# Optimization experiments

Measured on AMD Instinct MI355X. Metric: run time of the kernel, lower is better.

## Reference

```python
import jax, jax.numpy as jnp
import numpy as np
from jax import lax

D_MODEL = 1024
D_STATE = 16
D_CONV = 4
EXPAND = 2
D_INNER = EXPAND * D_MODEL  # 2048
DT_RANK = (D_MODEL + 15) // 16  # 64
EPS = 1e-5


def setup_inputs() -> dict:
    key = jax.random.key(0)
    ks = jax.random.split(key, 10)
    B, L = 2, 2048
    x = jax.random.normal(ks[0], (B, L, D_MODEL), dtype=jnp.float32)
    s = 0.02
    W_in = jax.random.normal(ks[1], (D_MODEL, 2 * D_INNER), dtype=jnp.float32) * s
    conv_w = jax.random.normal(ks[2], (D_INNER, 1, D_CONV), dtype=jnp.float32) * 0.3
    conv_b = jnp.zeros((D_INNER,), dtype=jnp.float32)
    W_xproj = jax.random.normal(ks[3], (D_INNER, DT_RANK + 2 * D_STATE), dtype=jnp.float32) * s
    W_dt = jax.random.normal(ks[4], (DT_RANK, D_INNER), dtype=jnp.float32) * s
    b_dt = jax.random.normal(ks[5], (D_INNER,), dtype=jnp.float32) * 0.1
    # canonical S4D-real init: A_log = log(1..d_state) broadcast over channels
    A_log = jnp.broadcast_to(jnp.log(jnp.arange(1, D_STATE + 1, dtype=jnp.float32)), (D_INNER, D_STATE))
    D = jnp.ones((D_INNER,), dtype=jnp.float32)
    W_out = jax.random.normal(ks[6], (D_INNER, D_MODEL), dtype=jnp.float32) * s
    return {
        'x': x,
        'ln_w': jnp.ones((D_MODEL,), dtype=jnp.float32),
        'ln_b': jnp.zeros((D_MODEL,), dtype=jnp.float32),
        'W_in': W_in, 'conv_w': conv_w, 'conv_b': conv_b,
        'W_xproj': W_xproj, 'W_dt': W_dt, 'b_dt': b_dt,
        'A_log': A_log, 'D': D, 'W_out': W_out,
    }


def _layernorm(x, w, b):
    mu = jnp.mean(x, axis=-1, keepdims=True)
    var = jnp.mean(jnp.square(x - mu), axis=-1, keepdims=True)
    return (x - mu) * lax.rsqrt(var + EPS) * w + b


def _mamba_forward(normed, W_in, conv_w, conv_b, W_xproj, W_dt, b_dt, A_log, D, W_out):
    Bsz, L, _ = normed.shape
    xz = normed @ W_in                       # (B, L, 2*d_inner)
    u, z = jnp.split(xz, 2, axis=-1)         # each (B, L, d_inner)
    # depthwise causal conv over time
    uc = lax.conv_general_dilated(
        jnp.swapaxes(u, 1, 2), conv_w,       # (B, d_inner, L), (d_inner, 1, k)
        window_strides=(1,), padding=[(D_CONV - 1, 0)],
        feature_group_count=D_INNER,
        dimension_numbers=('NCH', 'OIH', 'NCH'))
    uc = uc + conv_b[None, :, None]
    u = jax.nn.silu(jnp.swapaxes(uc, 1, 2))  # (B, L, d_inner)
    # input-dependent dt, B, C
    dbc = u @ W_xproj                        # (B, L, dt_rank + 2*d_state)
    dt = dbc[..., :DT_RANK]
    Bm = dbc[..., DT_RANK:DT_RANK + D_STATE]
    Cm = dbc[..., DT_RANK + D_STATE:]
    delta = jax.nn.softplus(dt @ W_dt + b_dt)  # (B, L, d_inner)
    A = -jnp.exp(A_log)                        # (d_inner, d_state)

    def step(h, inp):
        delta_t, u_t, B_t, C_t = inp           # (B,d), (B,d), (B,n), (B,n)
        dA = jnp.exp(delta_t[:, :, None] * A)  # (B, d, n)
        h = dA * h + (delta_t * u_t)[:, :, None] * B_t[:, None, :]
        y = jnp.einsum('bdn,bn->bd', h, C_t)
        return h, y

    tm = lambda a: jnp.swapaxes(a, 0, 1)       # time-major
    h0 = jnp.zeros((Bsz, D_INNER, D_STATE), dtype=normed.dtype)
    _, ys = lax.scan(step, h0, (tm(delta), tm(u), tm(Bm), tm(Cm)))
    y = jnp.swapaxes(ys, 0, 1) + u * D         # (B, L, d_inner)
    y = y * jax.nn.silu(z)
    return y @ W_out                            # (B, L, d_model)


def reference(x, ln_w, ln_b, W_in, conv_w, conv_b, W_xproj, W_dt, b_dt, A_log, D, W_out):
    normed = _layernorm(x, ln_w, ln_b)
    ssm_out = _mamba_forward(normed, W_in, conv_w, conv_b, W_xproj, W_dt, b_dt, A_log, D, W_out)
    # dropout is identity at inference
    return x + ssm_out
```

## Files before the change

### kernel.cpp

```cpp
#include <hip/hip_runtime.h>
#include <math.h>

#define D_MODEL 1024
#define D_INNER 2048
#define D_STATE 16
#define DT_RANK 64
#define LSEQ    2048
#define NTOK    4096
#define SCH     32
#define SCL     (LSEQ / SCH)
#define LOG2E   1.44269504088896f

typedef short bf16x8 __attribute__((ext_vector_type(8)));
typedef float f32x4  __attribute__((ext_vector_type(4)));

__device__ __forceinline__ unsigned bf16_rne(float v) {
    unsigned u = __float_as_uint(v);
    return (u + 0x7FFFu + ((u >> 16) & 1u)) >> 16;
}
__device__ __forceinline__ void split_hi_lo(float v, short& h, short& l) {
    unsigned hb = bf16_rne(v);
    h = (short)hb;
    float r = v - __uint_as_float(hb << 16);
    l = (short)bf16_rne(r);
}

__global__ __launch_bounds__(256) void ln_kernel(const float* __restrict__ x,
                                                 const float* __restrict__ w,
                                                 const float* __restrict__ b,
                                                 short* __restrict__ nh,
                                                 short* __restrict__ nl)
{
    int t = blockIdx.x;
    const float4* xr = (const float4*)(x + (size_t)t * D_MODEL);
    float4 v = xr[threadIdx.x];
    float s  = v.x + v.y + v.z + v.w;
    float s2 = v.x*v.x + v.y*v.y + v.z*v.z + v.w*v.w;
    for (int off = 32; off > 0; off >>= 1) {
        s  += __shfl_down(s, off);
        s2 += __shfl_down(s2, off);
    }
    __shared__ float red[8];
    int wid = threadIdx.x >> 6, lane = threadIdx.x & 63;
    if (lane == 0) { red[wid] = s; red[4 + wid] = s2; }
    __syncthreads();
    if (threadIdx.x == 0) {
        float a = red[0] + red[1] + red[2] + red[3];
        float c = red[4] + red[5] + red[6] + red[7];
        red[0] = a * (1.f / (float)D_MODEL);
        red[4] = c * (1.f / (float)D_MODEL);
    }
    __syncthreads();
    float mu  = red[0];
    float var = red[4] - mu * mu;
    float rs  = rsqrtf(var + 1e-5f);
    float4 wv = ((const float4*)w)[threadIdx.x];
    float4 bv = ((const float4*)b)[threadIdx.x];
    float4 o;
    o.x = (v.x - mu) * rs * wv.x + bv.x;
    o.y = (v.y - mu) * rs * wv.y + bv.y;
    o.z = (v.z - mu) * rs * wv.z + bv.z;
    o.w = (v.w - mu) * rs * wv.w + bv.w;
    short4 h4, l4;
    split_hi_lo(o.x, h4.x, l4.x);
    split_hi_lo(o.y, h4.y, l4.y);
    split_hi_lo(o.z, h4.z, l4.z);
    split_hi_lo(o.w, h4.w, l4.w);
    size_t off = (size_t)t * D_MODEL + threadIdx.x * 4;
    *(short4*)&nh[off] = h4;
    *(short4*)&nl[off] = l4;
}

__global__ __launch_bounds__(256) void cvtT_k(const float* __restrict__ W,
                                              short* __restrict__ Th,
                                              short* __restrict__ Tl,
                                              int R, int Cc)
{
    __shared__ float t[64][65];
    int rr = threadIdx.x >> 4;
    int cc = (threadIdx.x & 15) << 2;
    int r0 = blockIdx.y * 64, c0 = blockIdx.x * 64;
#pragma unroll
    for (int s = 0; s < 4; ++s) {
        float4 v = *(const float4*)&W[(size_t)(r0 + rr + 16*s) * Cc + c0 + cc];
        t[rr+16*s][cc+0] = v.x; t[rr+16*s][cc+1] = v.y;
        t[rr+16*s][cc+2] = v.z; t[rr+16*s][cc+3] = v.w;
    }
    __syncthreads();
#pragma unroll
    for (int s = 0; s < 4; ++s) {
        int orow = rr + 16*s;
        short4 h4, l4;
        split_hi_lo(t[cc+0][orow], h4.x, l4.x);
        split_hi_lo(t[cc+1][orow], h4.y, l4.y);
        split_hi_lo(t[cc+2][orow], h4.z, l4.z);
        split_hi_lo(t[cc+3][orow], h4.w, l4.w);
        size_t off = (size_t)(c0 + orow) * R + r0 + cc;
        *(short4*)&Th[off] = h4;
        *(short4*)&Tl[off] = l4;
    }
}

template<int EPI>
__global__ __launch_bounds__(256) void mgemm_k(const short* __restrict__ Ah,
                                               const short* __restrict__ Al,
                                               const short* __restrict__ Bh,
                                               const short* __restrict__ Bl,
                                               float* __restrict__ C, int ldc,
                                               int K, const float* __restrict__ aux)
{
    __shared__ short lds[4][128 * 32];

    int tid  = threadIdx.x;
    int w    = tid >> 6;
    int lane = tid & 63;
    int wr   = w >> 1, wc = w & 1;
    int row0 = blockIdx.y * 128;
    int col0 = blockIdx.x * 128;

    const short* gA = (w & 1) ? Al : Ah;
    const short* gB = (w & 1) ? Bl : Bh;
    const short* g  = (w & 2) ? gB : gA;
    int obase       = (w & 2) ? col0 : row0;
    const short* gtile = g + (size_t)obase * K;

    int srow  = lane >> 2;
    int skc   = lane & 3;
    int swoff = skc * 128 + srow * 8;

    int fr = lane & 15;
    int kg = lane >> 4;

    f32x4 acc[4][4] = {};

    for (int k0 = 0; k0 < K; k0 += 32) {
        bf16x8 stg[8];
#pragma unroll
        for (int i = 0; i < 8; ++i)
            stg[i] = *(const bf16x8*)(gtile + (size_t)(i * 16 + srow) * K + k0 + skc * 8);
        __syncthreads();
#pragma unroll
        for (int i = 0; i < 8; ++i)
            *(bf16x8*)&lds[w][i * 512 + swoff] = stg[i];
        __syncthreads();

        bf16x8 a_h[4], a_l[4], b_h[4], b_l[4];
#pragma unroll
        for (int m = 0; m < 4; ++m) {
            int ra = ((wr * 4 + m) * 4 + kg) * 128 + fr * 8;
            int rb = ((wc * 4 + m) * 4 + kg) * 128 + fr * 8;
            a_h[m] = *(const bf16x8*)&lds[0][ra];
            a_l[m] = *(const bf16x8*)&lds[1][ra];
            b_h[m] = *(const bf16x8*)&lds[2][rb];
            b_l[m] = *(const bf16x8*)&lds[3][rb];
        }
#pragma unroll
        for (int m = 0; m < 4; ++m)
#pragma unroll
            for (int n = 0; n < 4; ++n)
                acc[m][n] = __builtin_amdgcn_mfma_f32_16x16x32_bf16(a_h[m], b_h[n], acc[m][n], 0, 0, 0);
#pragma unroll
        for (int m = 0; m < 4; ++m)
#pragma unroll
            for (int n = 0; n < 4; ++n)
                acc[m][n] = __builtin_amdgcn_mfma_f32_16x16x32_bf16(a_l[m], b_h[n], acc[m][n], 0, 0, 0);
#pragma unroll
        for (int m = 0; m < 4; ++m)
#pragma unroll
            for (int n = 0; n < 4; ++n)
                acc[m][n] = __builtin_amdgcn_mfma_f32_16x16x32_bf16(a_h[m], b_l[n], acc[m][n], 0, 0, 0);
    }

#pragma unroll
    for (int m = 0; m < 4; ++m) {
        int row = row0 + wr * 64 + m * 16 + kg * 4;
#pragma unroll
        for (int n = 0; n < 4; ++n) {
            int col = col0 + wc * 64 + n * 16 + fr;
#pragma unroll
            for (int j = 0; j < 4; ++j) {
                size_t off = (size_t)(row + j) * ldc + col;
                float v = acc[m][n][j];
                if (EPI == 2) v += aux[off];
                C[off] = v;
            }
        }
    }
}

#define TBM 128
#define TBN 128
#define TBK 16

template<int EPI>
__global__ __launch_bounds__(256) void sgemm128_k(const float* __restrict__ A, int lda,
                                                  const float* __restrict__ B, int ldb,
                                                  float* __restrict__ C, int ldc,
                                                  int K, const float* __restrict__ aux)
{
    __shared__ float As[TBK][TBM + 4];
    __shared__ float Bs[TBK][TBN + 4];

    int tid  = threadIdx.x;
    int row0 = blockIdx.y * TBM;
    int col0 = blockIdx.x * TBN;

    int arow = tid >> 2;
    int acol = (tid & 3) << 2;
    int brow = tid >> 5;
    int bcol = (tid & 31) << 2;

    int tr = tid >> 4;
    int tc = tid & 15;

    float acc[8][8] = {};

    for (int k0 = 0; k0 < K; k0 += TBK) {
        float4 a0 = *(const float4*)(A + (size_t)(row0 + arow)      * lda + k0 + acol);
        float4 a1 = *(const float4*)(A + (size_t)(row0 + arow + 64) * lda + k0 + acol);
        float4 b0 = *(const float4*)(B + (size_t)(k0 + brow)     * ldb + col0 + bcol);
        float4 b1 = *(const float4*)(B + (size_t)(k0 + brow + 8) * ldb + col0 + bcol);
        __syncthreads();
        As[acol + 0][arow] = a0.x;
        As[acol + 1][arow] = a0.y;
        As[acol + 2][arow] = a0.z;
        As[acol + 3][arow] = a0.w;
        As[acol + 0][arow + 64] = a1.x;
        As[acol + 1][arow + 64] = a1.y;
        As[acol + 2][arow + 64] = a1.z;
        As[acol + 3][arow + 64] = a1.w;
        *(float4*)&Bs[brow][bcol]     = b0;
        *(float4*)&Bs[brow + 8][bcol] = b1;
        __syncthreads();
#pragma unroll
        for (int kk = 0; kk < TBK; ++kk) {
            float4 x0 = *(const float4*)&As[kk][tr << 2];
            float4 x1 = *(const float4*)&As[kk][(tr << 2) + 64];
            float4 y0 = *(const float4*)&Bs[kk][tc << 2];
            float4 y1 = *(const float4*)&Bs[kk][(tc << 2) + 64];
            float xa[8] = {x0.x, x0.y, x0.z, x0.w, x1.x, x1.y, x1.z, x1.w};
            float yb[8] = {y0.x, y0.y, y0.z, y0.w, y1.x, y1.y, y1.z, y1.w};
#pragma unroll
            for (int i = 0; i < 8; ++i)
#pragma unroll
                for (int j = 0; j < 8; ++j)
                    acc[i][j] = fmaf(xa[i], yb[j], acc[i][j]);
        }
    }

#pragma unroll
    for (int ih = 0; ih < 2; ++ih) {
#pragma unroll
        for (int i = 0; i < 4; ++i) {
            int r = row0 + (tr << 2) + ih * 64 + i;
#pragma unroll
            for (int jh = 0; jh < 2; ++jh) {
                int c = col0 + (tc << 2) + jh * 64;
                size_t off = (size_t)r * ldc + c;
                float4 v = *(const float4*)&acc[ih * 4 + i][jh * 4];
                if (EPI == 1) {
                    float4 bb = *(const float4*)(aux + c);
                    float t0;
                    t0 = v.x + bb.x; v.x = fmaxf(t0, 0.f) + log1pf(expf(-fabsf(t0)));
                    t0 = v.y + bb.y; v.y = fmaxf(t0, 0.f) + log1pf(expf(-fabsf(t0)));
                    t0 = v.z + bb.z; v.z = fmaxf(t0, 0.f) + log1pf(expf(-fabsf(t0)));
                    t0 = v.w + bb.w; v.w = fmaxf(t0, 0.f) + log1pf(expf(-fabsf(t0)));
                } else if (EPI == 2) {
                    float4 rr = *(const float4*)(aux + off);
                    v.x += rr.x; v.y += rr.y; v.z += rr.z; v.w += rr.w;
                }
                *(float4*)(C + off) = v;
            }
        }
    }
}

#define GBM 64
#define GBN 64
#define GBK 16

__global__ __launch_bounds__(256) void sgemm64_k(const float* __restrict__ A, int lda,
                                                 const float* __restrict__ B, int ldb,
                                                 float* __restrict__ C, int ldc,
                                                 int N, int K)
{
    __shared__ float As[GBK][GBM + 4];
    __shared__ float Bs[GBK][GBN + 4];

    int tid  = threadIdx.x;
    int row0 = blockIdx.y * GBM;
    int col0 = blockIdx.x * GBN;

    int ar = tid >> 2;
    int ac = (tid & 3) << 2;
    int br = tid >> 4;
    int bc = (tid & 15) << 2;

    int tr = tid >> 4;
    int tc = tid & 15;

    float acc[4][4] = {};

    for (int k0 = 0; k0 < K; k0 += GBK) {
        float4 av = *(const float4*)(A + (size_t)(row0 + ar) * lda + k0 + ac);
        float4 bv;
        int gcol = col0 + bc;
        if (gcol + 3 < N) {
            bv = *(const float4*)(B + (size_t)(k0 + br) * ldb + gcol);
        } else {
            const float* brow_p = B + (size_t)(k0 + br) * ldb;
            bv.x = (gcol + 0 < N) ? brow_p[gcol + 0] : 0.f;
            bv.y = (gcol + 1 < N) ? brow_p[gcol + 1] : 0.f;
            bv.z = (gcol + 2 < N) ? brow_p[gcol + 2] : 0.f;
            bv.w = (gcol + 3 < N) ? brow_p[gcol + 3] : 0.f;
        }
        __syncthreads();
        As[ac + 0][ar] = av.x;
        As[ac + 1][ar] = av.y;
        As[ac + 2][ar] = av.z;
        As[ac + 3][ar] = av.w;
        *(float4*)&Bs[br][bc] = bv;
        __syncthreads();
#pragma unroll
        for (int kk = 0; kk < GBK; ++kk) {
            float4 a = *(const float4*)&As[kk][tr << 2];
            float4 b = *(const float4*)&Bs[kk][tc << 2];
            acc[0][0] += a.x * b.x; acc[0][1] += a.x * b.y; acc[0][2] += a.x * b.z; acc[0][3] += a.x * b.w;
            acc[1][0] += a.y * b.x; acc[1][1] += a.y * b.y; acc[1][2] += a.y * b.z; acc[1][3] += a.y * b.w;
            acc[2][0] += a.z * b.x; acc[2][1] += a.z * b.y; acc[2][2] += a.z * b.z; acc[2][3] += a.z * b.w;
            acc[3][0] += a.w * b.x; acc[3][1] += a.w * b.y; acc[3][2] += a.w * b.z; acc[3][3] += a.w * b.w;
        }
    }

    int r0 = row0 + (tr << 2);
    int c0 = col0 + (tc << 2);
#pragma unroll
    for (int i = 0; i < 4; ++i) {
#pragma unroll
        for (int j = 0; j < 4; ++j) {
            int c = c0 + j;
            if (c < N) C[(size_t)(r0 + i) * ldc + c] = acc[i][j];
        }
    }
}

__global__ __launch_bounds__(256) void conv_silu_kernel(const float* __restrict__ xz,
                                                        const float* __restrict__ conv_w,
                                                        const float* __restrict__ conv_b,
                                                        float* __restrict__ uc)
{
    int idx = blockIdx.x * 256 + threadIdx.x;
    if (idx >= NTOK * D_INNER) return;
    int d  = idx & (D_INNER - 1);
    int bl = idx >> 11;
    int l  = bl & (LSEQ - 1);
    float4 w = ((const float4*)conv_w)[d];
    float acc = conv_b[d];
    if (l >= 3) acc += w.x * xz[(size_t)(bl - 3) * (2 * D_INNER) + d];
    if (l >= 2) acc += w.y * xz[(size_t)(bl - 2) * (2 * D_INNER) + d];
    if (l >= 1) acc += w.z * xz[(size_t)(bl - 1) * (2 * D_INNER) + d];
    acc += w.w * xz[(size_t)bl * (2 * D_INNER) + d];
    uc[idx] = acc / (1.f + expf(-acc));
}

__global__ __launch_bounds__(256) void scan1_kernel(const float* __restrict__ delta,
                                                    const float* __restrict__ uc,
                                                    const float* __restrict__ dbc,
                                                    const float* __restrict__ A_log,
                                                    float* __restrict__ carry_A,
                                                    float* __restrict__ carry_h)
{
    __shared__ float Bs[SCL][16];
    int tid = threadIdx.x;
    int chunk = blockIdx.x, dg = blockIdx.y, b = blockIdx.z;
    int d = dg * 256 + tid;
    int rb0 = b * LSEQ + chunk * SCL;

    for (int i = tid; i < SCL * 16; i += 256) {
        int l = i >> 4, n = i & 15;
        Bs[l][n] = dbc[(size_t)(rb0 + l) * 96 + DT_RANK + n];
    }
    __syncthreads();

    float A2[16];
#pragma unroll
    for (int q = 0; q < 4; ++q) {
        float4 a = *(const float4*)&A_log[d * D_STATE + q * 4];
        A2[q*4+0] = -expf(a.x) * LOG2E;
        A2[q*4+1] = -expf(a.y) * LOG2E;
        A2[q*4+2] = -expf(a.z) * LOG2E;
        A2[q*4+3] = -expf(a.w) * LOG2E;
    }

    float h[16];
#pragma unroll
    for (int n = 0; n < 16; ++n) h[n] = 0.f;
    float sdv = 0.f;

    const float* dp = delta + (size_t)rb0 * D_INNER + d;
    const float* up = uc    + (size_t)rb0 * D_INNER + d;

    float dv = dp[0], uv = up[0];
    for (int l = 0; l < SCL; ++l) {
        float dvn = 0.f, uvn = 0.f;
        if (l + 1 < SCL) { dvn = dp[(l+1) * D_INNER]; uvn = up[(l+1) * D_INNER]; }
        float du = dv * uv;
        sdv += dv;
#pragma unroll
        for (int q = 0; q < 4; ++q) {
            float4 bq = *(const float4*)&Bs[l][q * 4];
            h[q*4+0] = fmaf(exp2f(dv * A2[q*4+0]), h[q*4+0], du * bq.x);
            h[q*4+1] = fmaf(exp2f(dv * A2[q*4+1]), h[q*4+1], du * bq.y);
            h[q*4+2] = fmaf(exp2f(dv * A2[q*4+2]), h[q*4+2], du * bq.z);
            h[q*4+3] = fmaf(exp2f(dv * A2[q*4+3]), h[q*4+3], du * bq.w);
        }
        dv = dvn; uv = uvn;
    }

    size_t cb = (((size_t)chunk * 2 + b) * D_INNER + d) * D_STATE;
#pragma unroll
    for (int q = 0; q < 4; ++q) {
        float4 ap, hh;
        ap.x = exp2f(sdv * A2[q*4+0]); ap.y = exp2f(sdv * A2[q*4+1]);
        ap.z = exp2f(sdv * A2[q*4+2]); ap.w = exp2f(sdv * A2[q*4+3]);
        hh.x = h[q*4+0]; hh.y = h[q*4+1]; hh.z = h[q*4+2]; hh.w = h[q*4+3];
        *(float4*)&carry_A[cb + q * 4] = ap;
        *(float4*)&carry_h[cb + q * 4] = hh;
    }
}

__global__ __launch_bounds__(256) void scan2_kernel(const float* __restrict__ carry_A,
                                                    float* __restrict__ carry_h)
{
    int idx = blockIdx.x * 256 + threadIdx.x;
    float h = 0.f;
#pragma unroll
    for (int c = 0; c < SCH; ++c) {
        size_t a = (size_t)c * (2 * D_INNER * D_STATE) + idx;
        float Ap = carry_A[a];
        float he = carry_h[a];
        carry_h[a] = h;
        h = fmaf(Ap, h, he);
    }
}

__global__ __launch_bounds__(256) void scan3_kernel(const float* __restrict__ delta,
                                                    const float* __restrict__ uc,
                                                    const float* __restrict__ dbc,
                                                    const float* __restrict__ xz,
                                                    const float* __restrict__ A_log,
                                                    const float* __restrict__ Dp,
                                                    const float* __restrict__ carry_h,
                                                    short* __restrict__ ygh,
                                                    short* __restrict__ ygl)
{
    __shared__ float Bs[SCL][16];
    __shared__ float Cs[SCL][16];
    int tid = threadIdx.x;
    int chunk = blockIdx.x, dg = blockIdx.y, b = blockIdx.z;
    int d = dg * 256 + tid;
    int rb0 = b * LSEQ + chunk * SCL;

    for (int i = tid; i < SCL * 32; i += 256) {
        int l = i >> 5, o = i & 31;
        float v = dbc[(size_t)(rb0 + l) * 96 + DT_RANK + o];
        if (o < 16) Bs[l][o] = v; else Cs[l][o - 16] = v;
    }
    __syncthreads();

    float A2[16];
#pragma unroll
    for (int q = 0; q < 4; ++q) {
        float4 a = *(const float4*)&A_log[d * D_STATE + q * 4];
        A2[q*4+0] = -expf(a.x) * LOG2E;
        A2[q*4+1] = -expf(a.y) * LOG2E;
        A2[q*4+2] = -expf(a.z) * LOG2E;
        A2[q*4+3] = -expf(a.w) * LOG2E;
    }
    float Dv = Dp[d];

    float h[16];
    size_t cb = (((size_t)chunk * 2 + b) * D_INNER + d) * D_STATE;
#pragma unroll
    for (int q = 0; q < 4; ++q) {
        float4 hh = *(const float4*)&carry_h[cb + q * 4];
        h[q*4+0] = hh.x; h[q*4+1] = hh.y; h[q*4+2] = hh.z; h[q*4+3] = hh.w;
    }

    const float* dp = delta + (size_t)rb0 * D_INNER + d;
    const float* up = uc    + (size_t)rb0 * D_INNER + d;
    const float* zp = xz    + (size_t)rb0 * (2 * D_INNER) + D_INNER + d;
    short* yhp = ygh + (size_t)rb0 * D_INNER + d;
    short* ylp = ygl + (size_t)rb0 * D_INNER + d;

    float dv = dp[0], uv = up[0], zv = zp[0];
    for (int l = 0; l < SCL; ++l) {
        float dvn = 0.f, uvn = 0.f, zvn = 0.f;
        if (l + 1 < SCL) {
            dvn = dp[(l+1) * D_INNER];
            uvn = up[(l+1) * D_INNER];
            zvn = zp[(size_t)(l+1) * (2 * D_INNER)];
        }
        float du = dv * uv;
        float y = 0.f;
#pragma unroll
        for (int q = 0; q < 4; ++q) {
            float4 bq = *(const float4*)&Bs[l][q * 4];
            float4 cq = *(const float4*)&Cs[l][q * 4];
            h[q*4+0] = fmaf(exp2f(dv * A2[q*4+0]), h[q*4+0], du * bq.x);
            h[q*4+1] = fmaf(exp2f(dv * A2[q*4+1]), h[q*4+1], du * bq.y);
            h[q*4+2] = fmaf(exp2f(dv * A2[q*4+2]), h[q*4+2], du * bq.z);
            h[q*4+3] = fmaf(exp2f(dv * A2[q*4+3]), h[q*4+3], du * bq.w);
            y = fmaf(h[q*4+0], cq.x, y);
            y = fmaf(h[q*4+1], cq.y, y);
            y = fmaf(h[q*4+2], cq.z, y);
            y = fmaf(h[q*4+3], cq.w, y);
        }
        float yd  = fmaf(uv, Dv, y);
        float val = yd * (zv / (1.f + expf(-zv)));
        short hh, ll;
        split_hi_lo(val, hh, ll);
        yhp[l * D_INNER] = hh;
        ylp[l * D_INNER] = ll;
        dv = dvn; uv = uvn; zv = zvn;
    }
}

__global__ __launch_bounds__(256) void scan_kernel(const float* __restrict__ delta,
                                                   const float* __restrict__ uc,
                                                   const float* __restrict__ dbc,
                                                   const float* __restrict__ xz,
                                                   const float* __restrict__ A_log,
                                                   const float* __restrict__ Dp,
                                                   short* __restrict__ ygh,
                                                   short* __restrict__ ygl)
{
    int tid = threadIdx.x;
    int g = tid >> 4, n = tid & 15;
    int bid = blockIdx.x;
    int b = bid >> 7;
    int d = (bid & 127) * 16 + g;
    float Adn = -expf(A_log[d * D_STATE + n]);
    float Dv  = Dp[d];
    float h = 0.f;
    size_t rowb = (size_t)b * LSEQ;

    float dv = delta[rowb * D_INNER + d];
    float uv = uc[rowb * D_INNER + d];
    float Bv = dbc[rowb * 96 + DT_RANK + n];
    float Cv = dbc[rowb * 96 + DT_RANK + D_STATE + n];

    for (int l = 0; l < LSEQ; ++l) {
        float dv_n = 0.f, uv_n = 0.f, Bv_n = 0.f, Cv_n = 0.f;
        if (l + 1 < LSEQ) {
            size_t r = rowb + l + 1;
            dv_n = delta[r * D_INNER + d];
            uv_n = uc[r * D_INNER + d];
            Bv_n = dbc[r * 96 + DT_RANK + n];
            Cv_n = dbc[r * 96 + DT_RANK + D_STATE + n];
        }
        float dA = expf(dv * Adn);
        h = fmaf(dA, h, dv * uv * Bv);
        float p = h * Cv;
        p += __shfl_xor(p, 1);
        p += __shfl_xor(p, 2);
        p += __shfl_xor(p, 4);
        p += __shfl_xor(p, 8);
        if (n == 0) {
            size_t r = rowb + l;
            float zv = xz[r * (2 * D_INNER) + D_INNER + d];
            float y  = fmaf(uv, Dv, p);
            float val = y * (zv / (1.f + expf(-zv)));
            short hh, ll;
            split_hi_lo(val, hh, ll);
            ygh[r * D_INNER + d] = hh;
            ygl[r * D_INNER + d] = ll;
        }
        dv = dv_n; uv = uv_n; Bv = Bv_n; Cv = Cv_n;
    }
}

extern "C" void kernel_launch(void* const* d_in, const int* in_sizes, int n_in,
                              void* d_out, int out_size, void* d_ws, size_t ws_size,
                              hipStream_t stream)
{
    const float* x      = (const float*)d_in[0];
    const float* ln_w   = (const float*)d_in[1];
    const float* ln_b   = (const float*)d_in[2];
    const float* W_in   = (const float*)d_in[3];
    const float* conv_w = (const float*)d_in[4];
    const float* conv_b = (const float*)d_in[5];
    const float* W_xprj = (const float*)d_in[6];
    const float* W_dt   = (const float*)d_in[7];
    const float* b_dt   = (const float*)d_in[8];
    const float* A_log  = (const float*)d_in[9];
    const float* Dp     = (const float*)d_in[10];
    const float* W_out  = (const float*)d_in[11];
    float* out = (float*)d_out;

    float* xz    = (float*)d_ws;
    float* uc    = xz    + (size_t)NTOK * 2 * D_INNER;
    float* dbc   = uc    + (size_t)NTOK * D_INNER;
    float* delta = dbc   + (size_t)NTOK * 96;
    short* s0    = (short*)(delta + (size_t)NTOK * D_INNER);
    short* nh    = s0;
    short* nl    = nh   + (size_t)NTOK * D_MODEL;
    short* wiTh  = nl   + (size_t)NTOK * D_MODEL;
    short* wiTl  = wiTh + (size_t)(2 * D_INNER) * D_MODEL;
    short* ygh   = s0;
    short* ygl   = ygh  + (size_t)NTOK * D_INNER;
    short* woTh  = ygl  + (size_t)NTOK * D_INNER;
    short* woTl  = woTh + (size_t)D_MODEL * D_INNER;
    float* carry_A = (float*)(s0 + (size_t)20971520);
    float* carry_h = carry_A + (size_t)2 * D_INNER * D_STATE * SCH;

    size_t needed_base = (size_t)135790592 + (size_t)41943040;
    size_t needed_fast = needed_base + (size_t)2 * 2 * D_INNER * D_STATE * SCH * 4;
    if (ws_size < needed_base) return;
    bool fast_scan = (ws_size >= needed_fast);

    cvtT_k<<<dim3(2 * D_INNER / 64, D_MODEL / 64), 256, 0, stream>>>(W_in, wiTh, wiTl, D_MODEL, 2 * D_INNER);
    cvtT_k<<<dim3(D_MODEL / 64, D_INNER / 64), 256, 0, stream>>>(W_out, woTh, woTl, D_INNER, D_MODEL);
    ln_kernel<<<NTOK, 256, 0, stream>>>(x, ln_w, ln_b, nh, nl);
    mgemm_k<0><<<dim3(2 * D_INNER / 128, NTOK / 128), 256, 0, stream>>>(
        nh, nl, wiTh, wiTl, xz, 2 * D_INNER, D_MODEL, nullptr);
    conv_silu_kernel<<<(NTOK * D_INNER) / 256, 256, 0, stream>>>(xz, conv_w, conv_b, uc);
    sgemm64_k<<<dim3(2, NTOK / GBM), 256, 0, stream>>>(
        uc, D_INNER, W_xprj, 96, dbc, 96, 96, D_INNER);
    sgemm128_k<1><<<dim3(D_INNER / TBN, NTOK / TBM), 256, 0, stream>>>(
        dbc, 96, W_dt, D_INNER, delta, D_INNER, DT_RANK, b_dt);
    if (fast_scan) {
        scan1_kernel<<<dim3(SCH, D_INNER / 256, 2), 256, 0, stream>>>(
            delta, uc, dbc, A_log, carry_A, carry_h);
        scan2_kernel<<<(2 * D_INNER * D_STATE) / 256, 256, 0, stream>>>(carry_A, carry_h);
        scan3_kernel<<<dim3(SCH, D_INNER / 256, 2), 256, 0, stream>>>(
            delta, uc, dbc, xz, A_log, Dp, carry_h, ygh, ygl);
    } else {
        scan_kernel<<<256, 256, 0, stream>>>(delta, uc, dbc, xz, A_log, Dp, ygh, ygl);
    }
    mgemm_k<2><<<dim3(D_MODEL / 128, NTOK / 128), 256, 0, stream>>>(
        ygh, ygl, woTh, woTl, out, D_MODEL, D_INNER, x);
}
```

Baseline: 639.3 us.

## Split-K x_proj GEMM with reduction kernel and direct global-to-LDS loads in mgemm

```diff
diff --git a/kernel.cpp b/kernel.cpp
--- a/kernel.cpp
+++ b/kernel.cpp
@@ -10,6 +10,8 @@
 #define SCH     32
 #define SCL     (LSEQ / SCH)
 #define LOG2E   1.44269504088896f
+#define XKS     4
+#define XKC     (D_INNER / XKS)
 
 typedef short bf16x8 __attribute__((ext_vector_type(8)));
 typedef float f32x4  __attribute__((ext_vector_type(4)));
@@ -124,16 +126,27 @@
     int obase       = (w & 2) ? col0 : row0;
     const short* gtile = g + (size_t)obase * K;
 
-    int srow  = lane >> 2;
-    int skc   = lane & 3;
-    int swoff = skc * 128 + srow * 8;
-
     int fr = lane & 15;
     int kg = lane >> 4;
 
     f32x4 acc[4][4] = {};
 
     for (int k0 = 0; k0 < K; k0 += 32) {
+#if __has_builtin(__builtin_amdgcn_global_load_lds)
+        __syncthreads();
+#pragma unroll
+        for (int i = 0; i < 8; ++i) {
+            const short* src = gtile + (size_t)(i * 16 + fr) * K + k0 + kg * 8;
+            __builtin_amdgcn_global_load_lds(
+                (const __attribute__((address_space(1))) void*)src,
+                (__attribute__((address_space(3))) void*)&lds[w][i * 512],
+                16, 0, 0);
+        }
+        __syncthreads();
+#else
+        int srow  = lane >> 2;
+        int skc   = lane & 3;
+        int swoff = skc * 128 + srow * 8;
         bf16x8 stg[8];
 #pragma unroll
         for (int i = 0; i < 8; ++i)
@@ -143,6 +156,7 @@
         for (int i = 0; i < 8; ++i)
             *(bf16x8*)&lds[w][i * 512 + swoff] = stg[i];
         __syncthreads();
+#endif
 
         bf16x8 a_h[4], a_l[4], b_h[4], b_l[4];
 #pragma unroll
@@ -275,73 +289,56 @@
     }
 }
 
-#define GBM 64
-#define GBN 64
-#define GBK 16
-
-__global__ __launch_bounds__(256) void sgemm64_k(const float* __restrict__ A, int lda,
-                                                 const float* __restrict__ B, int ldb,
-                                                 float* __restrict__ C, int ldc,
-                                                 int N, int K)
-{
-    __shared__ float As[GBK][GBM + 4];
-    __shared__ float Bs[GBK][GBN + 4];
-
-    int tid  = threadIdx.x;
-    int row0 = blockIdx.y * GBM;
-    int col0 = blockIdx.x * GBN;
-
-    int ar = tid >> 2;
-    int ac = (tid & 3) << 2;
-    int br = tid >> 4;
-    int bc = (tid & 15) << 2;
-
-    int tr = tid >> 4;
-    int tc = tid & 15;
-
-    float acc[4][4] = {};
-
-    for (int k0 = 0; k0 < K; k0 += GBK) {
-        float4 av = *(const float4*)(A + (size_t)(row0 + ar) * lda + k0 + ac);
-        float4 bv;
-        int gcol = col0 + bc;
-        if (gcol + 3 < N) {
-            bv = *(const float4*)(B + (size_t)(k0 + br) * ldb + gcol);
-        } else {
-            const float* brow_p = B + (size_t)(k0 + br) * ldb;
-            bv.x = (gcol + 0 < N) ? brow_p[gcol + 0] : 0.f;
-            bv.y = (gcol + 1 < N) ? brow_p[gcol + 1] : 0.f;
-            bv.z = (gcol + 2 < N) ? brow_p[gcol + 2] : 0.f;
-            bv.w = (gcol + 3 < N) ? brow_p[gcol + 3] : 0.f;
-        }
-        __syncthreads();
-        As[ac + 0][ar] = av.x;
-        As[ac + 1][ar] = av.y;
-        As[ac + 2][ar] = av.z;
-        As[ac + 3][ar] = av.w;
-        *(float4*)&Bs[br][bc] = bv;
-        __syncthreads();
-#pragma unroll
-        for (int kk = 0; kk < GBK; ++kk) {
-            float4 a = *(const float4*)&As[kk][tr << 2];
-            float4 b = *(const float4*)&Bs[kk][tc << 2];
-            acc[0][0] += a.x * b.x; acc[0][1] += a.x * b.y; acc[0][2] += a.x * b.z; acc[0][3] += a.x * b.w;
-            acc[1][0] += a.y * b.x; acc[1][1] += a.y * b.y; acc[1][2] += a.y * b.z; acc[1][3] += a.y * b.w;
-            acc[2][0] += a.z * b.x; acc[2][1] += a.z * b.y; acc[2][2] += a.z * b.z; acc[2][3] += a.z * b.w;
-            acc[3][0] += a.w * b.x; acc[3][1] += a.w * b.y; acc[3][2] += a.w * b.z; acc[3][3] += a.w * b.w;
-        }
-    }
-
-    int r0 = row0 + (tr << 2);
-    int c0 = col0 + (tc << 2);
-#pragma unroll
-    for (int i = 0; i < 4; ++i) {
-#pragma unroll
-        for (int j = 0; j < 4; ++j) {
-            int c = c0 + j;
-            if (c < N) C[(size_t)(r0 + i) * ldc + c] = acc[i][j];
-        }
-    }
+__global__ __launch_bounds__(256) void xproj_k(const float* __restrict__ A,
+                                               const float* __restrict__ W,
+                                               float* __restrict__ part)
+{
+    int row = blockIdx.x * 256 + threadIdx.x;
+    int cg  = blockIdx.y;
+    int ks  = blockIdx.z;
+    const float4* a4 = (const float4*)(A + (size_t)row * D_INNER + ks * XKC);
+    const float* w = W + (size_t)ks * XKC * 96 + cg * 8;
+    float acc[8] = {};
+#pragma unroll 2
+    for (int k4 = 0; k4 < XKC / 4; ++k4) {
+        float4 av = a4[k4];
+        const float* wk = w + (size_t)k4 * 4 * 96;
+        float a0 = av.x, a1 = av.y, a2 = av.z, a3 = av.w;
+#pragma unroll
+        for (int kk = 0; kk < 4; ++kk) {
+            float ak = (kk == 0) ? a0 : (kk == 1) ? a1 : (kk == 2) ? a2 : a3;
+            float4 w0 = *(const float4*)(wk + (size_t)kk * 96);
+            float4 w1 = *(const float4*)(wk + (size_t)kk * 96 + 4);
+            acc[0] = fmaf(ak, w0.x, acc[0]);
+            acc[1] = fmaf(ak, w0.y, acc[1]);
+            acc[2] = fmaf(ak, w0.z, acc[2]);
+            acc[3] = fmaf(ak, w0.w, acc[3]);
+            acc[4] = fmaf(ak, w1.x, acc[4]);
+            acc[5] = fmaf(ak, w1.y, acc[5]);
+            acc[6] = fmaf(ak, w1.z, acc[6]);
+            acc[7] = fmaf(ak, w1.w, acc[7]);
+        }
+    }
+    float* p = part + ((size_t)ks * NTOK + row) * 96 + cg * 8;
+    *(float4*)p       = *(float4*)&acc[0];
+    *(float4*)(p + 4) = *(float4*)&acc[4];
+}
+
+__global__ __launch_bounds__(256) void xreduce_k(const float* __restrict__ part,
+                                                 float* __restrict__ dbc)
+{
+    int i = blockIdx.x * 256 + threadIdx.x;
+    const float4* p = (const float4*)part;
+    float4 s0 = p[i];
+    float4 s1 = p[i + 98304];
+    float4 s2 = p[i + 2 * 98304];
+    float4 s3 = p[i + 3 * 98304];
+    float4 s;
+    s.x = (s0.x + s1.x) + (s2.x + s3.x);
+    s.y = (s0.y + s1.y) + (s2.y + s3.y);
+    s.z = (s0.z + s1.z) + (s2.z + s3.z);
+    s.w = (s0.w + s1.w) + (s2.w + s3.w);
+    ((float4*)dbc)[i] = s;
 }
 
 __global__ __launch_bounds__(256) void conv_silu_kernel(const float* __restrict__ xz,
@@ -611,6 +608,7 @@
     short* ygl   = ygh  + (size_t)NTOK * D_INNER;
     short* woTh  = ygl  + (size_t)NTOK * D_INNER;
     short* woTl  = woTh + (size_t)D_MODEL * D_INNER;
+    float* xpart = (float*)s0;
     float* carry_A = (float*)(s0 + (size_t)20971520);
     float* carry_h = carry_A + (size_t)2 * D_INNER * D_STATE * SCH;
 
@@ -625,8 +623,8 @@
     mgemm_k<0><<<dim3(2 * D_INNER / 128, NTOK / 128), 256, 0, stream>>>(
         nh, nl, wiTh, wiTl, xz, 2 * D_INNER, D_MODEL, nullptr);
     conv_silu_kernel<<<(NTOK * D_INNER) / 256, 256, 0, stream>>>(xz, conv_w, conv_b, uc);
-    sgemm64_k<<<dim3(2, NTOK / GBM), 256, 0, stream>>>(
-        uc, D_INNER, W_xprj, 96, dbc, 96, 96, D_INNER);
+    xproj_k<<<dim3(NTOK / 256, 12, XKS), 256, 0, stream>>>(uc, W_xprj, xpart);
+    xreduce_k<<<(NTOK * 96 / 4) / 256, 256, 0, stream>>>(xpart, dbc);
     sgemm128_k<1><<<dim3(D_INNER / TBN, NTOK / TBM), 256, 0, stream>>>(
         dbc, 96, W_dt, D_INNER, delta, D_INNER, DT_RANK, b_dt);
     if (fast_scan) {
```

Measured after the change: 599.0 us. 6.3% less time.
